# Kernel optimization log

Hardware: AMD Instinct MI355X
Metric: run time of the kernel (lower is better)

Reference implementation:

```python
import jax, jax.numpy as jnp
import numpy as np

N = 50000   # nodes
E = 800000  # edges (before self loops)
G = 8       # graphs in batch
IN, H, HD = 3, 64, 128


def setup_inputs() -> dict:
    key = jax.random.key(0)
    ks = jax.random.split(key, 12)
    s = 0.1  # weight scale
    return {
        "x": jax.random.normal(ks[0], (N, IN), jnp.float32),
        "edge_index": jax.random.randint(ks[1], (2, E), 0, N, dtype=jnp.int32),
        "batch": jnp.sort(jax.random.randint(ks[2], (N,), 0, G, dtype=jnp.int32)),
        "W1": s * jax.random.normal(ks[3], (IN, H), jnp.float32),
        "a_src1": s * jax.random.normal(ks[4], (H,), jnp.float32),
        "a_dst1": s * jax.random.normal(ks[5], (H,), jnp.float32),
        "b1": jnp.zeros((H,), jnp.float32),
        "W2": s * jax.random.normal(ks[6], (H, H), jnp.float32),
        "a_src2": s * jax.random.normal(ks[7], (H,), jnp.float32),
        "a_dst2": s * jax.random.normal(ks[8], (H,), jnp.float32),
        "b2": jnp.zeros((H,), jnp.float32),
        "Wh1": s * jax.random.normal(ks[9], (H, HD), jnp.float32),
        "bh1": jnp.zeros((HD,), jnp.float32),
        "Wh2": s * jax.random.normal(ks[10], (HD, 1), jnp.float32),
        "bh2": jnp.zeros((1,), jnp.float32),
    }


def gat_conv(x, src, dst, W, a_src, a_dst, b, n_nodes):
    """Single-head GATConv (PyG defaults: slope 0.2, self-loops, bias)."""
    h = x @ W                           # [N, H]
    e_s = h @ a_src                     # [N] per-node source logits
    e_d = h @ a_dst                     # [N] per-node target logits
    e = jax.nn.leaky_relu(e_s[src] + e_d[dst], 0.2)  # [E']
    # segment softmax over incoming edges of each target node
    m = jax.ops.segment_max(e, dst, num_segments=n_nodes)
    ex = jnp.exp(e - m[dst])
    denom = jax.ops.segment_sum(ex, dst, num_segments=n_nodes)
    alpha = ex / denom[dst]             # [E']
    out = jax.ops.segment_sum(h[src] * alpha[:, None], dst, num_segments=n_nodes)
    return out + b


def reference(x, edge_index, batch, W1, a_src1, a_dst1, b1,
              W2, a_src2, a_dst2, b2, Wh1, bh1, Wh2, bh2):
    n = x.shape[0]
    loops = jnp.arange(n, dtype=edge_index.dtype)
    src = jnp.concatenate([edge_index[0], loops])  # add self loops
    dst = jnp.concatenate([edge_index[1], loops])

    h = jax.nn.relu(gat_conv(x, src, dst, W1, a_src1, a_dst1, b1, n))
    h = jax.nn.relu(gat_conv(h, src, dst, W2, a_src2, a_dst2, b2, n))

    # global mean pool per graph
    sums = jax.ops.segment_sum(h, batch, num_segments=G)          # [G, H]
    cnt = jax.ops.segment_sum(jnp.ones((n,), h.dtype), batch, num_segments=G)
    pooled = sums / jnp.maximum(cnt, 1.0)[:, None]

    # value head: Linear -> ReLU -> Linear
    return jax.nn.relu(pooled @ Wh1 + bh1) @ Wh2 + bh2            # [G, 1]
```

## Files before the change

kernel.cpp:

```cpp
#include <hip/hip_runtime.h>
#include <math.h>

#define NN 50000
#define NE 800000
#define NG 8
#define H 64
#define HD 128
#define CAP 48
#define NSLICE 64
#define NPART 8
#define PART_SZ (NN / NPART)
#define EPT 8
#define ETH (NE / EPT)
#define ECHUNKS ((ETH + 255) / 256)
#define SCB (ECHUNKS * NPART)
#define NODEB ((NN * H) / 256)

typedef unsigned short ushort_t;
typedef _Float16 half_t;
typedef _Float16 half2_t __attribute__((ext_vector_type(2)));
typedef int int4v __attribute__((ext_vector_type(4)));

#define SCAT(dv, sv)                                                             \
    {                                                                            \
        if ((dv) / PART_SZ == part) {                                            \
            int slot = atomicAdd(&deg[dv], 1);                                   \
            if (slot < CAP) csr[(size_t)(dv) * CAP + slot] = (ushort_t)(sv);     \
        }                                                                        \
    }

__global__ void k_sc_n1(const int* __restrict__ src, const int* __restrict__ dst,
                        int* __restrict__ deg, ushort_t* __restrict__ csr,
                        const float* __restrict__ x, const float* __restrict__ W,
                        const float* __restrict__ asrc, const float* __restrict__ adst,
                        const float* __restrict__ W2, half2_t* __restrict__ W2p,
                        half_t* __restrict__ h, float* __restrict__ es, float* __restrict__ ed) {
    int bid = blockIdx.x;
    if (bid < SCB) {
        int part = bid & (NPART - 1);
        int t = (bid >> 3) * 256 + threadIdx.x;
        int e0 = t * EPT;
        if (e0 < NE) {
            int4v da = __builtin_nontemporal_load((const int4v*)(dst + e0));
            int4v db = __builtin_nontemporal_load((const int4v*)(dst + e0 + 4));
            bool any = (da.x / PART_SZ == part) | (da.y / PART_SZ == part) |
                       (da.z / PART_SZ == part) | (da.w / PART_SZ == part) |
                       (db.x / PART_SZ == part) | (db.y / PART_SZ == part) |
                       (db.z / PART_SZ == part) | (db.w / PART_SZ == part);
            if (any) {
                int4v sa = __builtin_nontemporal_load((const int4v*)(src + e0));
                int4v sb = __builtin_nontemporal_load((const int4v*)(src + e0 + 4));
                SCAT(da.x, sa.x) SCAT(da.y, sa.y) SCAT(da.z, sa.z) SCAT(da.w, sa.w)
                SCAT(db.x, sb.x) SCAT(db.y, sb.y) SCAT(db.z, sb.z) SCAT(db.w, sb.w)
            }
        }
    } else if (bid < SCB + NODEB) {
        int nid = (bid - SCB) * 256 + threadIdx.x;
        int node = nid >> 6, lane = nid & 63;
        if (node >= NN) return;
        float x0 = x[node*3+0], x1 = x[node*3+1], x2 = x[node*3+2];
        float hv = x0*W[lane] + x1*W[64+lane] + x2*W[128+lane];
        __builtin_nontemporal_store((half_t)hv, h + (size_t)node*64 + lane);
        float s = hv * asrc[lane], d = hv * adst[lane];
        #pragma unroll
        for (int o = 32; o > 0; o >>= 1) { s += __shfl_xor(s, o); d += __shfl_xor(d, o); }
        if (lane == 0) { es[node] = s; ed[node] = d; }
    } else {
        for (int i = threadIdx.x; i < (H/2) * 64; i += 256) {
            int k2 = i >> 6, ln = i & 63;
            half2_t v;
            v.x = (_Float16)W2[(2*k2)*64 + ln];
            v.y = (_Float16)W2[(2*k2+1)*64 + ln];
            W2p[i] = v;
        }
    }
}


#define GSETUP(S, nodeS)                                                         \
    int n##S = deg[nodeS]; n##S = n##S > CAP ? CAP : n##S;                       \
    float edn##S = ed[nodeS];                                                    \
    float hself##S = (float)hH[(size_t)(nodeS)*64 + lane];                       \
    int s0##S = 0; float ev##S = -1e30f;                                         \
    if (lane < n##S) {                                                           \
        s0##S = csr[(size_t)(nodeS) * CAP + lane];                               \
        float e0 = es[s0##S] + edn##S;                                           \
        ev##S = e0 > 0.f ? e0 : 0.2f * e0;                                       \
    }                                                                            \
    float evs##S = es[nodeS] + edn##S;                                           \
    evs##S = evs##S > 0.f ? evs##S : 0.2f * evs##S;

#define CHUNK(S, ci, accv)                                                       \
    {                                                                            \
        int r = (ci) * 4 + sub;                                                  \
        float q = (r < n##S) ? sp##S[r] : 0.f;                                   \
        int idx = (r < n##S) ? sidx##S[r] : 0;                                   \
        float2 raw = *(const float2*)(hH + (size_t)idx * 64 + c4);               \
        union { float2 f; half_t hh[4]; } u; u.f = raw;                          \
        accv.x += (float)u.hh[0] * q; accv.y += (float)u.hh[1] * q;              \
        accv.z += (float)u.hh[2] * q; accv.w += (float)u.hh[3] * q;              \
    }

#define REDIST(S)                                                                \
    float chs##S;                                                                \
    {                                                                            \
        int srcl = lane >> 2;                                                    \
        float v0 = __shfl(a##S.x, srcl);                                         \
        float v1 = __shfl(a##S.y, srcl);                                         \
        float v2 = __shfl(a##S.z, srcl);                                         \
        float v3 = __shfl(a##S.w, srcl);                                         \
        int j = lane & 3;                                                        \
        chs##S = (j == 0) ? v0 : (j == 1) ? v1 : (j == 2) ? v2 : v3;             \
    }

#define GATHER_BODY                                                              \
    GSETUP(A, ndA) GSETUP(B, ndB)                                                \
    float mA = fmaxf(evA, evsA), mB = fmaxf(evB, evsB);                          \
    _Pragma("unroll")                                                            \
    for (int o = 32; o > 0; o >>= 1) {                                           \
        mA = fmaxf(mA, __shfl_xor(mA, o));                                       \
        mB = fmaxf(mB, __shfl_xor(mB, o));                                       \
    }                                                                            \
    float pA = (lane < nA) ? __expf(evA - mA) : 0.f;                             \
    float pB = (lane < nB) ? __expf(evB - mB) : 0.f;                             \
    float sumA = pA, sumB = pB;                                                  \
    _Pragma("unroll")                                                            \
    for (int o = 32; o > 0; o >>= 1) {                                           \
        sumA += __shfl_xor(sumA, o);                                             \
        sumB += __shfl_xor(sumB, o);                                             \
    }                                                                            \
    float psA = __expf(evsA - mA), psB = __expf(evsB - mB);                      \
    float invA = 1.0f / (sumA + psA), invB = 1.0f / (sumB + psB);                \
    sidxA[lane] = s0A; spA[lane] = pA;                                           \
    sidxB[lane] = s0B; spB[lane] = pB;                                           \
    int sub = lane >> 4;                                                         \
    int c4  = (lane & 15) * 4;                                                   \
    float4 aA = {0,0,0,0}, aA1 = {0,0,0,0}, aB = {0,0,0,0}, aB1 = {0,0,0,0};     \
    int nmax = nA > nB ? nA : nB;                                                \
    int nch = (nmax + 3) >> 2;                                                   \
    int k = 0;                                                                   \
    for (; k + 2 <= nch; k += 2) {                                               \
        CHUNK(A, k, aA) CHUNK(B, k, aB) CHUNK(A, k+1, aA1) CHUNK(B, k+1, aB1)    \
    }                                                                            \
    for (; k < nch; ++k) { CHUNK(A, k, aA) CHUNK(B, k, aB) }                     \
    aA.x += aA1.x; aA.y += aA1.y; aA.z += aA1.z; aA.w += aA1.w;                  \
    aB.x += aB1.x; aB.y += aB1.y; aB.z += aB1.z; aB.w += aB1.w;                  \
    _Pragma("unroll")                                                            \
    for (int o = 16; o <= 32; o <<= 1) {                                         \
        aA.x += __shfl_xor(aA.x, o); aA.y += __shfl_xor(aA.y, o);                \
        aA.z += __shfl_xor(aA.z, o); aA.w += __shfl_xor(aA.w, o);                \
        aB.x += __shfl_xor(aB.x, o); aB.y += __shfl_xor(aB.y, o);                \
        aB.z += __shfl_xor(aB.z, o); aB.w += __shfl_xor(aB.w, o);                \
    }                                                                            \
    REDIST(A) REDIST(B)                                                          \
    float fA = fmaxf((chsA + psA * hselfA) * invA + bl, 0.f);                    \
    float fB = fmaxf((chsB + psB * hselfB) * invB + bl, 0.f);

__global__ void k_gather1(const int* __restrict__ deg, const ushort_t* __restrict__ csr,
                          const float* __restrict__ es, const float* __restrict__ ed,
                          const half_t* __restrict__ hH, const float* __restrict__ b,
                          const half2_t* __restrict__ W2p, const float* __restrict__ as2,
                          const float* __restrict__ ad2,
                          half_t* __restrict__ h2, float* __restrict__ es2,
                          float* __restrict__ ed2) {
    __shared__ int   s_idx[4][2][64];
    __shared__ float s_p[4][2][64];
    __shared__ half2_t s_fh[4][2][32];
    int lane = threadIdx.x & 63, w = threadIdx.x >> 6;
    int wv = blockIdx.x * 4 + w;
    int ndA = wv * 2, ndB = ndA + 1;
    int*   sidxA = s_idx[w][0]; int*   sidxB = s_idx[w][1];
    float* spA   = s_p[w][0];   float* spB   = s_p[w][1];
    float bl = b[lane], as2l = as2[lane], ad2l = ad2[lane];

    GATHER_BODY

    ((half_t*)s_fh[w][0])[lane] = (half_t)fA;
    ((half_t*)s_fh[w][1])[lane] = (half_t)fB;
    float hvA = 0.f, hvB = 0.f;
    #pragma unroll
    for (int k2 = 0; k2 < 32; ++k2) {
        half2_t w2v = W2p[k2*64 + lane];
        half2_t fa2 = s_fh[w][0][k2];
        half2_t fb2 = s_fh[w][1][k2];
#if __has_builtin(__builtin_amdgcn_fdot2)
        hvA = __builtin_amdgcn_fdot2(fa2, w2v, hvA, false);
        hvB = __builtin_amdgcn_fdot2(fb2, w2v, hvB, false);
#else
        hvA += (float)fa2.x * (float)w2v.x + (float)fa2.y * (float)w2v.y;
        hvB += (float)fb2.x * (float)w2v.x + (float)fb2.y * (float)w2v.y;
#endif
    }
    h2[(size_t)ndA*64 + lane] = (half_t)hvA;
    h2[(size_t)ndB*64 + lane] = (half_t)hvB;
    float ssA = hvA * as2l, ddA = hvA * ad2l;
    float ssB = hvB * as2l, ddB = hvB * ad2l;
    #pragma unroll
    for (int o = 32; o > 0; o >>= 1) {
        ssA += __shfl_xor(ssA, o); ddA += __shfl_xor(ddA, o);
        ssB += __shfl_xor(ssB, o); ddB += __shfl_xor(ddB, o);
    }
    if (lane == 0) { es2[ndA] = ssA; ed2[ndA] = ddA; es2[ndB] = ssB; ed2[ndB] = ddB; }
}

__global__ void k_gather2(const int* __restrict__ deg, const ushort_t* __restrict__ csr,
                          const float* __restrict__ es, const float* __restrict__ ed,
                          const half_t* __restrict__ hH, const float* __restrict__ b,
                          const int* __restrict__ batch,
                          float* __restrict__ sums, float* __restrict__ cnt) {
    __shared__ int   s_idx[4][2][64];
    __shared__ float s_p[4][2][64];
    __shared__ float part[NG * H];
    __shared__ float pc[NG];
    for (int i = threadIdx.x; i < NG * H; i += 256) part[i] = 0.f;
    if (threadIdx.x < NG) pc[threadIdx.x] = 0.f;
    __syncthreads();

    int lane = threadIdx.x & 63, w = threadIdx.x >> 6;
    int wv = blockIdx.x * 4 + w;
    int ndA = wv * 2, ndB = ndA + 1;
    int*   sidxA = s_idx[w][0]; int*   sidxB = s_idx[w][1];
    float* spA   = s_p[w][0];   float* spB   = s_p[w][1];
    float bl = b[lane];

    GATHER_BODY

    int gA = batch[ndA], gB = batch[ndB];
    atomicAdd(&part[gA * H + lane], fA);
    atomicAdd(&part[gB * H + lane], fB);
    if (lane == 0) { atomicAdd(&pc[gA], 1.f); atomicAdd(&pc[gB], 1.f); }
    __syncthreads();
    int slice = blockIdx.x & (NSLICE - 1);
    float* ssum = sums + (size_t)slice * (NG * H);
    float* scnt = cnt + (size_t)slice * NG;
    for (int i = threadIdx.x; i < NG * H; i += 256) atomicAdd(&ssum[i], part[i]);
    if (threadIdx.x < NG) atomicAdd(&scnt[threadIdx.x], pc[threadIdx.x]);
}

__global__ void k_head(const float* __restrict__ sums, const float* __restrict__ cnt,
                       const float* __restrict__ Wh1, const float* __restrict__ bh1,
                       const float* __restrict__ Wh2, const float* __restrict__ bh2,
                       float* __restrict__ out) {
    __shared__ float pooled[NG * H];
    __shared__ float hidden[NG * HD];
    __shared__ float c_s[NG];
    int t = threadIdx.x;
    if (t < NG) {
        float c = 0.f;
        for (int s = 0; s < NSLICE; ++s) c += cnt[s * NG + t];
        c_s[t] = fmaxf(c, 1.f);
    }
    __syncthreads();
    for (int i = t; i < NG * H; i += blockDim.x) {
        float v = 0.f;
        for (int s = 0; s < NSLICE; ++s) v += sums[(size_t)s * (NG * H) + i];
        pooled[i] = v / c_s[i >> 6];
    }
    __syncthreads();
    for (int i = t; i < NG * HD; i += blockDim.x) {
        int g = i / HD, hd = i % HD;
        float acc = bh1[hd];
        for (int c = 0; c < H; ++c) acc += pooled[g * H + c] * Wh1[c * HD + hd];
        hidden[i] = fmaxf(acc, 0.f);
    }
    __syncthreads();
    if (t < NG) {
        float acc = bh2[0];
        for (int hd = 0; hd < HD; ++hd) acc += hidden[t * HD + hd] * Wh2[hd];
        out[t] = acc;
    }
}

extern "C" void kernel_launch(void* const* d_in, const int* in_sizes, int n_in,
                              void* d_out, int out_size, void* d_ws, size_t ws_size,
                              hipStream_t stream) {
    const float* x    = (const float*)d_in[0];
    const int*   ei   = (const int*)d_in[1];
    const int*   batch= (const int*)d_in[2];
    const float* W1   = (const float*)d_in[3];
    const float* as1  = (const float*)d_in[4];
    const float* ad1  = (const float*)d_in[5];
    const float* b1   = (const float*)d_in[6];
    const float* W2   = (const float*)d_in[7];
    const float* as2  = (const float*)d_in[8];
    const float* ad2  = (const float*)d_in[9];
    const float* b2   = (const float*)d_in[10];
    const float* Wh1  = (const float*)d_in[11];
    const float* bh1  = (const float*)d_in[12];
    const float* Wh2  = (const float*)d_in[13];
    const float* bh2  = (const float*)d_in[14];
    const int* src = ei;
    const int* dst = ei + NE;

    float* ws   = (float*)d_ws;
    half_t* h1  = (half_t*)ws;
    half_t* h2  = (half_t*)(ws + (size_t)NN*32);
    float* es1  = ws + (size_t)NN*64;
    float* ed1  = es1 + NN;
    float* es2  = ed1 + NN;
    float* ed2  = es2 + NN;
    int*   deg  = (int*)(ed2 + NN);
    float* sums = (float*)(deg + NN);
    float* cnt  = sums + (size_t)NSLICE*NG*H;
    ushort_t* csr = (ushort_t*)(cnt + NSLICE*NG);
    half2_t* W2p  = (half2_t*)(csr + (size_t)NN*CAP);

    size_t zeroBytes = (size_t)NN*4 + (size_t)NSLICE*NG*H*4 + (size_t)NSLICE*NG*4;

    dim3 blk(256);
    int scBlocks  = SCB + NODEB + 1;
    int gBlocks   = NN / 8;

    (void)hipMemsetAsync(deg, 0, zeroBytes, stream);
    k_sc_n1<<<scBlocks, blk, 0, stream>>>(src, dst, deg, csr, x, W1, as1, ad1,
                                          W2, W2p, h1, es1, ed1);
    k_gather1<<<gBlocks, blk, 0, stream>>>(deg, csr, es1, ed1, h1, b1, W2p, as2, ad2,
                                           h2, es2, ed2);
    k_gather2<<<gBlocks, blk, 0, stream>>>(deg, csr, es2, ed2, h2, b2, batch, sums, cnt);
    k_head<<<1, 256, 0, stream>>>(sums, cnt, Wh1, bh1, Wh2, bh2, (float*)d_out);
}
```

Measured before the change: 145.9 us.

## Gather one node per wavefront with fixed unrolled chunks and max-free softmax

Each wavefront now processes one node instead of two, and the grid doubles to cover all nodes. The softmax no longer subtracts the per-node max, which removes two wave-wide max reductions. The softmax denominator is now summed inside the gather loop. The gather loop is fully unrolled over all CAP/4 chunks with four independent accumulators, loading index 0 with zero weight for unused slots. This trades dynamic trip counts and two-node interleaving for more waves and fixed memory-level parallelism, but it issues redundant loads for low-degree nodes and risks exp overflow without max subtraction.

```diff
diff --git a/kernel.cpp b/kernel.cpp
--- a/kernel.cpp
+++ b/kernel.cpp
@@ -7,6 +7,7 @@
 #define H 64
 #define HD 128
 #define CAP 48
+#define NCHUNK (CAP / 4)
 #define NSLICE 64
 #define NPART 8
 #define PART_SZ (NN / NPART)
@@ -76,85 +77,61 @@
     }
 }
 
-
-#define GSETUP(S, nodeS)                                                         \
-    int n##S = deg[nodeS]; n##S = n##S > CAP ? CAP : n##S;                       \
-    float edn##S = ed[nodeS];                                                    \
-    float hself##S = (float)hH[(size_t)(nodeS)*64 + lane];                       \
-    int s0##S = 0; float ev##S = -1e30f;                                         \
-    if (lane < n##S) {                                                           \
-        s0##S = csr[(size_t)(nodeS) * CAP + lane];                               \
-        float e0 = es[s0##S] + edn##S;                                           \
-        ev##S = e0 > 0.f ? e0 : 0.2f * e0;                                       \
-    }                                                                            \
-    float evs##S = es[nodeS] + edn##S;                                           \
-    evs##S = evs##S > 0.f ? evs##S : 0.2f * evs##S;
-
-#define CHUNK(S, ci, accv)                                                       \
-    {                                                                            \
-        int r = (ci) * 4 + sub;                                                  \
-        float q = (r < n##S) ? sp##S[r] : 0.f;                                   \
-        int idx = (r < n##S) ? sidx##S[r] : 0;                                   \
+#define GATHER_CORE                                                              \
+    int n = deg[node]; n = n > CAP ? CAP : n;                                    \
+    float edn = ed[node], esn = es[node];                                        \
+    float hself = (float)hH[(size_t)node*64 + lane];                             \
+    int s0 = 0; float p0 = 0.f;                                                  \
+    if (lane < n) {                                                              \
+        s0 = csr[(size_t)node * CAP + lane];                                     \
+        float e0 = es[s0] + edn;                                                 \
+        e0 = e0 > 0.f ? e0 : 0.2f * e0;                                          \
+        p0 = __expf(e0);                                                         \
+    }                                                                            \
+    float evs = esn + edn; evs = evs > 0.f ? evs : 0.2f * evs;                   \
+    float ps = __expf(evs);                                                      \
+    sidx[lane] = s0; sp[lane] = p0;                                              \
+    int sub = lane >> 4;                                                         \
+    int c4  = (lane & 15) * 4;                                                   \
+    float4 acc[4];                                                               \
+    acc[0] = {0,0,0,0}; acc[1] = {0,0,0,0}; acc[2] = {0,0,0,0}; acc[3] = {0,0,0,0}; \
+    float dq = 0.f;                                                              \
+    _Pragma("unroll")                                                            \
+    for (int c = 0; c < NCHUNK; ++c) {                                           \
+        int r = c * 4 + sub;                                                     \
+        float q = (r < n) ? sp[r] : 0.f;                                         \
+        int idx = (r < n) ? sidx[r] : 0;                                         \
         float2 raw = *(const float2*)(hH + (size_t)idx * 64 + c4);               \
         union { float2 f; half_t hh[4]; } u; u.f = raw;                          \
-        accv.x += (float)u.hh[0] * q; accv.y += (float)u.hh[1] * q;              \
-        accv.z += (float)u.hh[2] * q; accv.w += (float)u.hh[3] * q;              \
-    }
-
-#define REDIST(S)                                                                \
-    float chs##S;                                                                \
+        acc[c & 3].x += (float)u.hh[0] * q;                                      \
+        acc[c & 3].y += (float)u.hh[1] * q;                                      \
+        acc[c & 3].z += (float)u.hh[2] * q;                                      \
+        acc[c & 3].w += (float)u.hh[3] * q;                                      \
+        dq += q;                                                                 \
+    }                                                                            \
+    float4 A;                                                                    \
+    A.x = acc[0].x + acc[1].x + acc[2].x + acc[3].x;                             \
+    A.y = acc[0].y + acc[1].y + acc[2].y + acc[3].y;                             \
+    A.z = acc[0].z + acc[1].z + acc[2].z + acc[3].z;                             \
+    A.w = acc[0].w + acc[1].w + acc[2].w + acc[3].w;                             \
+    _Pragma("unroll")                                                            \
+    for (int o = 16; o <= 32; o <<= 1) {                                         \
+        A.x += __shfl_xor(A.x, o); A.y += __shfl_xor(A.y, o);                    \
+        A.z += __shfl_xor(A.z, o); A.w += __shfl_xor(A.w, o);                    \
+        dq  += __shfl_xor(dq, o);                                                \
+    }                                                                            \
+    float inv = 1.0f / (dq + ps);                                                \
+    float chs;                                                                   \
     {                                                                            \
         int srcl = lane >> 2;                                                    \
-        float v0 = __shfl(a##S.x, srcl);                                         \
-        float v1 = __shfl(a##S.y, srcl);                                         \
-        float v2 = __shfl(a##S.z, srcl);                                         \
-        float v3 = __shfl(a##S.w, srcl);                                         \
+        float v0 = __shfl(A.x, srcl);                                            \
+        float v1 = __shfl(A.y, srcl);                                            \
+        float v2 = __shfl(A.z, srcl);                                            \
+        float v3 = __shfl(A.w, srcl);                                            \
         int j = lane & 3;                                                        \
-        chs##S = (j == 0) ? v0 : (j == 1) ? v1 : (j == 2) ? v2 : v3;             \
-    }
-
-#define GATHER_BODY                                                              \
-    GSETUP(A, ndA) GSETUP(B, ndB)                                                \
-    float mA = fmaxf(evA, evsA), mB = fmaxf(evB, evsB);                          \
-    _Pragma("unroll")                                                            \
-    for (int o = 32; o > 0; o >>= 1) {                                           \
-        mA = fmaxf(mA, __shfl_xor(mA, o));                                       \
-        mB = fmaxf(mB, __shfl_xor(mB, o));                                       \
-    }                                                                            \
-    float pA = (lane < nA) ? __expf(evA - mA) : 0.f;                             \
-    float pB = (lane < nB) ? __expf(evB - mB) : 0.f;                             \
-    float sumA = pA, sumB = pB;                                                  \
-    _Pragma("unroll")                                                            \
-    for (int o = 32; o > 0; o >>= 1) {                                           \
-        sumA += __shfl_xor(sumA, o);                                             \
-        sumB += __shfl_xor(sumB, o);                                             \
-    }                                                                            \
-    float psA = __expf(evsA - mA), psB = __expf(evsB - mB);                      \
-    float invA = 1.0f / (sumA + psA), invB = 1.0f / (sumB + psB);                \
-    sidxA[lane] = s0A; spA[lane] = pA;                                           \
-    sidxB[lane] = s0B; spB[lane] = pB;                                           \
-    int sub = lane >> 4;                                                         \
-    int c4  = (lane & 15) * 4;                                                   \
-    float4 aA = {0,0,0,0}, aA1 = {0,0,0,0}, aB = {0,0,0,0}, aB1 = {0,0,0,0};     \
-    int nmax = nA > nB ? nA : nB;                                                \
-    int nch = (nmax + 3) >> 2;                                                   \
-    int k = 0;                                                                   \
-    for (; k + 2 <= nch; k += 2) {                                               \
-        CHUNK(A, k, aA) CHUNK(B, k, aB) CHUNK(A, k+1, aA1) CHUNK(B, k+1, aB1)    \
-    }                                                                            \
-    for (; k < nch; ++k) { CHUNK(A, k, aA) CHUNK(B, k, aB) }                     \
-    aA.x += aA1.x; aA.y += aA1.y; aA.z += aA1.z; aA.w += aA1.w;                  \
-    aB.x += aB1.x; aB.y += aB1.y; aB.z += aB1.z; aB.w += aB1.w;                  \
-    _Pragma("unroll")                                                            \
-    for (int o = 16; o <= 32; o <<= 1) {                                         \
-        aA.x += __shfl_xor(aA.x, o); aA.y += __shfl_xor(aA.y, o);                \
-        aA.z += __shfl_xor(aA.z, o); aA.w += __shfl_xor(aA.w, o);                \
-        aB.x += __shfl_xor(aB.x, o); aB.y += __shfl_xor(aB.y, o);                \
-        aB.z += __shfl_xor(aB.z, o); aB.w += __shfl_xor(aB.w, o);                \
-    }                                                                            \
-    REDIST(A) REDIST(B)                                                          \
-    float fA = fmaxf((chsA + psA * hselfA) * invA + bl, 0.f);                    \
-    float fB = fmaxf((chsB + psB * hselfB) * invB + bl, 0.f);
+        chs = (j == 0) ? v0 : (j == 1) ? v1 : (j == 2) ? v2 : v3;                \
+    }                                                                            \
+    float f = fmaxf((chs + ps * hself) * inv + bl, 0.f);
 
 __global__ void k_gather1(const int* __restrict__ deg, const ushort_t* __restrict__ csr,
                           const float* __restrict__ es, const float* __restrict__ ed,
@@ -163,44 +140,36 @@
                           const float* __restrict__ ad2,
                           half_t* __restrict__ h2, float* __restrict__ es2,
                           float* __restrict__ ed2) {
-    __shared__ int   s_idx[4][2][64];
-    __shared__ float s_p[4][2][64];
-    __shared__ half2_t s_fh[4][2][32];
+    __shared__ int     s_idx[4][64];
+    __shared__ float   s_p[4][64];
+    __shared__ half2_t s_fh[4][32];
     int lane = threadIdx.x & 63, w = threadIdx.x >> 6;
-    int wv = blockIdx.x * 4 + w;
-    int ndA = wv * 2, ndB = ndA + 1;
-    int*   sidxA = s_idx[w][0]; int*   sidxB = s_idx[w][1];
-    float* spA   = s_p[w][0];   float* spB   = s_p[w][1];
+    int node = blockIdx.x * 4 + w;
+    int*   sidx = s_idx[w];
+    float* sp   = s_p[w];
     float bl = b[lane], as2l = as2[lane], ad2l = ad2[lane];
 
-    GATHER_BODY
-
-    ((half_t*)s_fh[w][0])[lane] = (half_t)fA;
-    ((half_t*)s_fh[w][1])[lane] = (half_t)fB;
-    float hvA = 0.f, hvB = 0.f;
+    GATHER_CORE
+
+    ((half_t*)s_fh[w])[lane] = (half_t)f;
+    float hv = 0.f;
     #pragma unroll
     for (int k2 = 0; k2 < 32; ++k2) {
         half2_t w2v = W2p[k2*64 + lane];
-        half2_t fa2 = s_fh[w][0][k2];
-        half2_t fb2 = s_fh[w][1][k2];
+        half2_t f2  = s_fh[w][k2];
 #if __has_builtin(__builtin_amdgcn_fdot2)
-        hvA = __builtin_amdgcn_fdot2(fa2, w2v, hvA, false);
-        hvB = __builtin_amdgcn_fdot2(fb2, w2v, hvB, false);
+        hv = __builtin_amdgcn_fdot2(f2, w2v, hv, false);
 #else
-        hvA += (float)fa2.x * (float)w2v.x + (float)fa2.y * (float)w2v.y;
-        hvB += (float)fb2.x * (float)w2v.x + (float)fb2.y * (float)w2v.y;
+        hv += (float)f2.x * (float)w2v.x + (float)f2.y * (float)w2v.y;
 #endif
     }
-    h2[(size_t)ndA*64 + lane] = (half_t)hvA;
-    h2[(size_t)ndB*64 + lane] = (half_t)hvB;
-    float ssA = hvA * as2l, ddA = hvA * ad2l;
-    float ssB = hvB * as2l, ddB = hvB * ad2l;
+    h2[(size_t)node*64 + lane] = (half_t)hv;
+    float ss = hv * as2l, dd = hv * ad2l;
     #pragma unroll
     for (int o = 32; o > 0; o >>= 1) {
-        ssA += __shfl_xor(ssA, o); ddA += __shfl_xor(ddA, o);
-        ssB += __shfl_xor(ssB, o); ddB += __shfl_xor(ddB, o);
-    }
-    if (lane == 0) { es2[ndA] = ssA; ed2[ndA] = ddA; es2[ndB] = ssB; ed2[ndB] = ddB; }
+        ss += __shfl_xor(ss, o); dd += __shfl_xor(dd, o);
+    }
+    if (lane == 0) { es2[node] = ss; ed2[node] = dd; }
 }
 
 __global__ void k_gather2(const int* __restrict__ deg, const ushort_t* __restrict__ csr,
@@ -208,8 +177,8 @@
                           const half_t* __restrict__ hH, const float* __restrict__ b,
                           const int* __restrict__ batch,
                           float* __restrict__ sums, float* __restrict__ cnt) {
-    __shared__ int   s_idx[4][2][64];
-    __shared__ float s_p[4][2][64];
+    __shared__ int   s_idx[4][64];
+    __shared__ float s_p[4][64];
     __shared__ float part[NG * H];
     __shared__ float pc[NG];
     for (int i = threadIdx.x; i < NG * H; i += 256) part[i] = 0.f;
@@ -217,18 +186,16 @@
     __syncthreads();
 
     int lane = threadIdx.x & 63, w = threadIdx.x >> 6;
-    int wv = blockIdx.x * 4 + w;
-    int ndA = wv * 2, ndB = ndA + 1;
-    int*   sidxA = s_idx[w][0]; int*   sidxB = s_idx[w][1];
-    float* spA   = s_p[w][0];   float* spB   = s_p[w][1];
+    int node = blockIdx.x * 4 + w;
+    int*   sidx = s_idx[w];
+    float* sp   = s_p[w];
     float bl = b[lane];
 
-    GATHER_BODY
-
-    int gA = batch[ndA], gB = batch[ndB];
-    atomicAdd(&part[gA * H + lane], fA);
-    atomicAdd(&part[gB * H + lane], fB);
-    if (lane == 0) { atomicAdd(&pc[gA], 1.f); atomicAdd(&pc[gB], 1.f); }
+    GATHER_CORE
+
+    int g = batch[node];
+    atomicAdd(&part[g * H + lane], f);
+    if (lane == 0) atomicAdd(&pc[g], 1.f);
     __syncthreads();
     int slice = blockIdx.x & (NSLICE - 1);
     float* ssum = sums + (size_t)slice * (NG * H);
@@ -309,7 +276,7 @@
 
     dim3 blk(256);
     int scBlocks  = SCB + NODEB + 1;
-    int gBlocks   = NN / 8;
+    int gBlocks   = NN / 4;
 
     (void)hipMemsetAsync(deg, 0, zeroBytes, stream);
     k_sc_n1<<<scBlocks, blk, 0, stream>>>(src, dst, deg, csr, x, W1, as1, ad1,
```

New measurement: 149.8 us. 1.03x slower.
